# Kernel tuning notes

Measured on AMD Instinct MI355X. Metric: run time of the kernel, lower is better.

Reference implementation:

```python
import jax, jax.numpy as jnp
import numpy as np

DIM = 180
HEADS = 6
HEAD_DIM = DIM // HEADS
SCALE = HEAD_DIM ** (-0.5)
BW, N, K = 8192, 64, 16


def setup_inputs() -> dict:
    key = jax.random.key(0)
    ks = jax.random.split(key, 6)
    return {
        "x": jax.random.normal(ks[0], (BW, N, DIM), dtype=jnp.float32),
        "bpe_windows": jax.random.normal(ks[1], (BW, N, K), dtype=jnp.float32),
        "qkv_w": jax.random.normal(ks[2], (3 * DIM, DIM), dtype=jnp.float32) * 0.05,
        "qkv_b": jax.random.normal(ks[3], (3 * DIM,), dtype=jnp.float32) * 0.05,
        "proj_w": jax.random.normal(ks[4], (DIM, DIM), dtype=jnp.float32) * 0.05,
        "proj_b": jax.random.normal(ks[5], (DIM,), dtype=jnp.float32) * 0.05,
        "tau": jnp.ones((HEADS, 1, 1), dtype=jnp.float32),
    }


def reference(x, bpe_windows, qkv_w, qkv_b, proj_w, proj_b, tau):
    B_, n, C = x.shape
    # qkv projection -> (3, B_, H, N, hd)
    qkv = (x @ qkv_w.T + qkv_b).reshape(B_, n, 3, HEADS, HEAD_DIM)
    qkv = jnp.transpose(qkv, (2, 0, 3, 1, 4))
    q, k, v = qkv[0], qkv[1], qkv[2]
    q = q * SCALE
    attn = jnp.einsum("bhid,bhjd->bhij", q, k)  # (B_, H, N, N)
    # geodesic bias from BPE embeddings: d_B(i,j) = ||bpe_i - bpe_j||_2
    diff = bpe_windows[:, :, None, :] - bpe_windows[:, None, :, :]  # (B_, N, N, K)
    d_B = jnp.sqrt(jnp.sum(diff * diff, axis=-1))  # (B_, N, N)
    log_W_geo = -d_B[:, None, :, :] / jnp.clip(tau, 1e-6)[None]  # (B_, H, N, N)
    attn = jax.nn.softmax(attn + log_W_geo, axis=-1)
    out = jnp.einsum("bhij,bhjd->bhid", attn, v)  # (B_, H, N, hd)
    out = jnp.transpose(out, (0, 2, 1, 3)).reshape(B_, n, C)
    return out @ proj_w.T + proj_b
```

## Files before the change

### kernel.cpp

```cpp
#include <hip/hip_runtime.h>
#include <hip/hip_fp16.h>
#include <math.h>

typedef __attribute__((ext_vector_type(8))) short short8b;
typedef __attribute__((ext_vector_type(4))) float f32x4;
typedef __attribute__((ext_vector_type(4))) unsigned short ushort4b;
typedef __attribute__((ext_vector_type(2))) unsigned short ushort2b;

#define NWIN 8192
#define NT   1024
#define SCALE 0.18257418583505536f

#define XB_P 200
#define QK_P 200
#define VT_P 72
#define DB_P 68
#define OFF_XB  0
#define OFF_QK  25600
#define OFF_VT  51200
#define OFF_DB  65024
#define OFF_BPE 73728
#define LDS_BYTES 78848

#define WK 192
#define ATT_P 184

__device__ __forceinline__ unsigned short f2bf(float f) {
    union { float f; unsigned int u; } v; v.f = f;
    return (unsigned short)((v.u + 0x7FFFu + ((v.u >> 16) & 1u)) >> 16);
}

__global__ void prep_weights(const float* __restrict__ qkv_w,
                             const float* __restrict__ proj_w,
                             unsigned short* __restrict__ wq2,
                             unsigned short* __restrict__ wp)
{
    const int idx = blockIdx.x * 256 + threadIdx.x;
    if (idx < 2 * 270 * WK) {
        const int p = idx / (270 * WK);
        const int rr = (idx / WK) % 270;
        const int kcol = idx % WK;
        const int which = rr / 90, hh = (rr % 90) / 30, dd = rr % 30;
        const int r_orig = which * 180 + (3 * p + hh) * 30 + dd;
        wq2[idx] = f2bf((kcol < 180) ? qkv_w[r_orig * 180 + kcol] : 0.f);
    }
    const int j = idx - 2 * 270 * WK;
    if (j >= 0 && j < WK * WK) {
        const int r = j / WK, c = j % WK;
        wp[j] = f2bf((r < 180 && c < 180) ? proj_w[r * 180 + c] : 0.f);
    }
}

__global__ void __launch_bounds__(NT, 8)
waga_mfma(const float* __restrict__ x,
          const float* __restrict__ bpe,
          const unsigned short* __restrict__ wq2,
          const unsigned short* __restrict__ wp,
          const float* __restrict__ qkv_b,
          const float* __restrict__ proj_b,
          const float* __restrict__ tau,
          float* __restrict__ out)
{
    extern __shared__ char smem[];
    unsigned short* xb   = (unsigned short*)(smem + OFF_XB);
    unsigned short* qk3  = (unsigned short*)(smem + OFF_QK);
    unsigned short* vT3  = (unsigned short*)(smem + OFF_VT);
    unsigned short* dBs  = (unsigned short*)(smem + OFF_DB);
    float*          bpes = (float*)(smem + OFF_BPE);

    const int b = blockIdx.x;
    const int t = threadIdx.x;
    const int w = t >> 6;
    const int l = t & 63;
    const int lr = l & 15;
    const int g  = l >> 4;

    unsigned short* attg = (unsigned short*)((char*)out + (size_t)b * 46080 + 22528);

    if (t < 192) {
        const int n = t / 3, c = t % 3;
        ushort4b z = {0, 0, 0, 0};
        *reinterpret_cast<ushort4b*>(xb + n * XB_P + 180 + 4 * c) = z;
    } else if (t < 576) {
        const int i = t - 192;
        const int n = i / 6, r = i % 6;
        const int col = (r >> 1) * 64 + (r & 1) * 32 + 30;
        ushort2b z2 = {0, 0};
        *reinterpret_cast<ushort2b*>(qk3 + n * QK_P + col) = z2;
    } else if (t < 640) {
        const int n = t - 576;
        ushort4b z = {0, 0, 0, 0};
        *reinterpret_cast<ushort4b*>(attg + n * ATT_P + 180) = z;
    }
    {
        const float* xw = x + (size_t)b * 11520;
        for (int i = t; i < 64 * 45; i += NT) {
            const int n = i / 45, c4 = i % 45;
            const float4 v = *reinterpret_cast<const float4*>(xw + i * 4);
            ushort4b o;
            o[0] = f2bf(v.x); o[1] = f2bf(v.y); o[2] = f2bf(v.z); o[3] = f2bf(v.w);
            *reinterpret_cast<ushort4b*>(xb + n * XB_P + c4 * 4) = o;
        }
    }
    if (t < 256) {
        const float4 v = *reinterpret_cast<const float4*>(bpe + (size_t)b * 1024 + t * 4);
        *reinterpret_cast<float4*>(bpes + (t >> 2) * 20 + (t & 3) * 4) = v;
    }
    __syncthreads();

    {
        const int ti = t >> 4, tj = t & 15;
        float acc[4] = {0.f, 0.f, 0.f, 0.f};
        #pragma unroll
        for (int k4 = 0; k4 < 4; ++k4) {
            const float4 a = *reinterpret_cast<const float4*>(bpes + ti * 20 + 4 * k4);
            #pragma unroll
            for (int e = 0; e < 4; ++e) {
                const float4 bb = *reinterpret_cast<const float4*>(bpes + (tj + 16 * e) * 20 + 4 * k4);
                float d;
                d = a.x - bb.x; acc[e] += d * d;
                d = a.y - bb.y; acc[e] += d * d;
                d = a.z - bb.z; acc[e] += d * d;
                d = a.w - bb.w; acc[e] += d * d;
            }
        }
        #pragma unroll
        for (int e = 0; e < 4; ++e)
            dBs[ti * DB_P + tj + 16 * e] =
                __half_as_ushort(__float2half_rn(sqrtf(acc[e])));
    }

    for (int pass = 0; pass < 2; ++pass) {
        if (pass) __syncthreads();

        const unsigned short* wqp = wq2 + (size_t)pass * 270 * WK;
        for (int tile = w; tile < 18; tile += 16) {
            const int seg = tile >> 1;
            const int which = seg / 3, hh = seg % 3;
            const int wbase = which * 90 + hh * 30;
            const int ddr = ((tile & 1) << 4) + lr;
            const bool arow_ok = (ddr < 30);
            const int ddb = ((tile & 1) << 4) + (g << 2);
            const int bbase = which * 180 + (3 * pass + hh) * 30 + ddb;
            float bias[4];
            #pragma unroll
            for (int i = 0; i < 4; ++i)
                bias[i] = (ddb + i < 30) ? qkv_b[bbase + i] : 0.f;
            f32x4 acc[4];
            #pragma unroll
            for (int mt = 0; mt < 4; ++mt) {
                acc[mt][0] = bias[0]; acc[mt][1] = bias[1];
                acc[mt][2] = bias[2]; acc[mt][3] = bias[3];
            }
            #pragma unroll
            for (int kk = 0; kk < 6; ++kk) {
                short8b af;
                if (arow_ok)
                    af = *reinterpret_cast<const short8b*>(
                        wqp + (size_t)(wbase + ddr) * WK + kk * 32 + g * 8);
                else
                    af = short8b{0,0,0,0,0,0,0,0};
                #pragma unroll
                for (int mt = 0; mt < 4; ++mt) {
                    const short8b bf = *reinterpret_cast<const short8b*>(
                        xb + (mt * 16 + lr) * XB_P + kk * 32 + g * 8);
                    acc[mt] = __builtin_amdgcn_mfma_f32_16x16x32_bf16(af, bf, acc[mt], 0, 0, 0);
                }
            }
            #pragma unroll
            for (int mt = 0; mt < 4; ++mt) {
                const int tok = mt * 16 + lr;
                float v0 = acc[mt][0], v1 = acc[mt][1], v2 = acc[mt][2], v3 = acc[mt][3];
                if (which == 0) { v0 *= SCALE; v1 *= SCALE; v2 *= SCALE; v3 *= SCALE; }
                if (which < 2) {
                    unsigned short* dst = qk3 + tok * QK_P + hh * 64 + which * 32 + ddb;
                    if (ddb < 28) {
                        ushort4b o = { f2bf(v0), f2bf(v1), f2bf(v2), f2bf(v3) };
                        *reinterpret_cast<ushort4b*>(dst) = o;
                    } else {
                        ushort2b o = { f2bf(v0), f2bf(v1) };
                        *reinterpret_cast<ushort2b*>(dst) = o;
                    }
                } else {
                    const int c = (tok & 32) + ((tok >> 2) & 3) * 8 + ((tok >> 4) & 1) * 4 + (tok & 3);
                    unsigned short* base = vT3 + hh * 2304 + c;
                    if (ddb + 0 < 30) base[(ddb + 0) * VT_P] = f2bf(v0);
                    if (ddb + 1 < 30) base[(ddb + 1) * VT_P] = f2bf(v1);
                    if (ddb + 2 < 30) base[(ddb + 2) * VT_P] = f2bf(v2);
                    if (ddb + 3 < 30) base[(ddb + 3) * VT_P] = f2bf(v3);
                }
            }
        }
        __syncthreads();

        if (w < 12) {
            const int hh = w >> 2, mt = w & 3;
            const int h = 3 * pass + hh;
            const float itau = 1.f / fmaxf(tau[h], 1e-6f);
            f32x4 s[4];
            #pragma unroll
            for (int jt = 0; jt < 4; ++jt)
                #pragma unroll
                for (int i = 0; i < 4; ++i) {
                    const float d = __half2float(__ushort_as_half(
                        dBs[(jt * 16 + g * 4 + i) * DB_P + mt * 16 + lr]));
                    s[jt][i] = -d * itau;
                }
            const short8b qf = *reinterpret_cast<const short8b*>(
                qk3 + (mt * 16 + lr) * QK_P + hh * 64 + g * 8);
            #pragma unroll
            for (int jt = 0; jt < 4; ++jt) {
                const short8b kf = *reinterpret_cast<const short8b*>(
                    qk3 + (jt * 16 + lr) * QK_P + hh * 64 + 32 + g * 8);
                s[jt] = __builtin_amdgcn_mfma_f32_16x16x32_bf16(kf, qf, s[jt], 0, 0, 0);
            }
            float mx = s[0][0];
            #pragma unroll
            for (int jt = 0; jt < 4; ++jt)
                #pragma unroll
                for (int i = 0; i < 4; ++i) mx = fmaxf(mx, s[jt][i]);
            mx = fmaxf(mx, __shfl_xor(mx, 16));
            mx = fmaxf(mx, __shfl_xor(mx, 32));
            float sum = 0.f;
            #pragma unroll
            for (int jt = 0; jt < 4; ++jt)
                #pragma unroll
                for (int i = 0; i < 4; ++i) {
                    const float p = __expf(s[jt][i] - mx);
                    s[jt][i] = p; sum += p;
                }
            sum += __shfl_xor(sum, 16);
            sum += __shfl_xor(sum, 32);
            const float inv = 1.f / sum;
            short8b pb[2];
            #pragma unroll
            for (int ks = 0; ks < 2; ++ks) {
                pb[ks][0] = (short)f2bf(s[2 * ks][0] * inv);
                pb[ks][1] = (short)f2bf(s[2 * ks][1] * inv);
                pb[ks][2] = (short)f2bf(s[2 * ks][2] * inv);
                pb[ks][3] = (short)f2bf(s[2 * ks][3] * inv);
                pb[ks][4] = (short)f2bf(s[2 * ks + 1][0] * inv);
                pb[ks][5] = (short)f2bf(s[2 * ks + 1][1] * inv);
                pb[ks][6] = (short)f2bf(s[2 * ks + 1][2] * inv);
                pb[ks][7] = (short)f2bf(s[2 * ks + 1][3] * inv);
            }
            const int tok = mt * 16 + lr;
            #pragma unroll
            for (int ntd = 0; ntd < 2; ++ntd) {
                f32x4 o = {0.f, 0.f, 0.f, 0.f};
                #pragma unroll
                for (int ks = 0; ks < 2; ++ks) {
                    const short8b va = *reinterpret_cast<const short8b*>(
                        vT3 + hh * 2304 + (ntd * 16 + lr) * VT_P + ks * 32 + g * 8);
                    o = __builtin_amdgcn_mfma_f32_16x16x32_bf16(va, pb[ks], o, 0, 0, 0);
                }
                const int col = h * 30 + ntd * 16 + g * 4;
                unsigned short* dst = attg + tok * ATT_P + col;
                if (ntd == 0 || g < 3) {
                    ushort4b ov = { f2bf(o[0]), f2bf(o[1]), f2bf(o[2]), f2bf(o[3]) };
                    *reinterpret_cast<ushort4b*>(dst) = ov;
                } else {
                    ushort2b ov = { f2bf(o[0]), f2bf(o[1]) };
                    *reinterpret_cast<ushort2b*>(dst) = ov;
                }
            }
        }
    }
    __syncthreads();

    f32x4 pacc[3];
    #pragma unroll
    for (int q3 = 0; q3 < 3; ++q3) {
        const int tid = 3 * w + q3;
        const int nt = tid >> 2, mt = tid & 3;
        f32x4 acc = {0.f, 0.f, 0.f, 0.f};
        #pragma unroll
        for (int kk = 0; kk < 6; ++kk) {
            short8b af;
            if (kk == 5 && g == 3)
                af = short8b{0,0,0,0,0,0,0,0};
            else
                af = *reinterpret_cast<const short8b*>(
                    attg + (mt * 16 + lr) * ATT_P + kk * 32 + g * 8);
            const short8b bf = *reinterpret_cast<const short8b*>(
                wp + (nt * 16 + lr) * WK + kk * 32 + g * 8);
            acc = __builtin_amdgcn_mfma_f32_16x16x32_bf16(af, bf, acc, 0, 0, 0);
        }
        pacc[q3] = acc;
    }
    __syncthreads();
    #pragma unroll
    for (int q3 = 0; q3 < 3; ++q3) {
        const int tid = 3 * w + q3;
        const int nt = tid >> 2, mt = tid & 3;
        const int chan = nt * 16 + lr;
        if (chan < 180) {
            const float pbv = proj_b[chan];
            #pragma unroll
            for (int i = 0; i < 4; ++i)
                out[((size_t)b * 64 + mt * 16 + g * 4 + i) * 180 + chan] = pacc[q3][i] + pbv;
        }
    }
}

extern "C" void kernel_launch(void* const* d_in, const int* in_sizes, int n_in,
                              void* d_out, int out_size, void* d_ws, size_t ws_size,
                              hipStream_t stream) {
    (void)in_sizes; (void)n_in; (void)out_size; (void)ws_size;
    const float* x      = (const float*)d_in[0];
    const float* bpe    = (const float*)d_in[1];
    const float* qkv_w  = (const float*)d_in[2];
    const float* qkv_b  = (const float*)d_in[3];
    const float* proj_w = (const float*)d_in[4];
    const float* proj_b = (const float*)d_in[5];
    const float* tau    = (const float*)d_in[6];

    unsigned short* wq2 = (unsigned short*)d_ws;
    unsigned short* wp  = wq2 + 2 * 270 * WK;

    prep_weights<<<(2 * 270 * WK + WK * WK + 255) / 256, 256, 0, stream>>>(
        qkv_w, proj_w, wq2, wp);

    (void)hipFuncSetAttribute((const void*)waga_mfma,
                              hipFuncAttributeMaxDynamicSharedMemorySize,
                              LDS_BYTES);
    waga_mfma<<<NWIN, NT, LDS_BYTES, stream>>>(x, bpe, wq2, wp, qkv_b, proj_b, tau,
                                               (float*)d_out);
}
```

Measured before the change: 799.7 us.

## Compute all six heads in one pass with LDS-resident attention output

Replaces the two-pass, three-heads-per-pass schedule with a single pass that projects Q/K/V for all six heads into a larger LDS buffer, removing one barrier round and the repeated work. The per-head attention output, previously spilled to the global output buffer as scratch, now goes into LDS (reusing the x buffer), and the projection weights are padded per head so the output projection reads 32-wide head slots directly. Weight and operand fragments are preloaded and double-buffered in registers, the distance matrix is kept in fp32, and final stores become float4. LDS grows from about 77KB to about 122KB, which cuts resident blocks per CU, and launch bounds change accordingly.

```diff
diff --git a/kernel.cpp b/kernel.cpp
--- a/kernel.cpp
+++ b/kernel.cpp
@@ -1,29 +1,27 @@
 #include <hip/hip_runtime.h>
-#include <hip/hip_fp16.h>
 #include <math.h>
 
 typedef __attribute__((ext_vector_type(8))) short short8b;
 typedef __attribute__((ext_vector_type(4))) float f32x4;
 typedef __attribute__((ext_vector_type(4))) unsigned short ushort4b;
-typedef __attribute__((ext_vector_type(2))) unsigned short ushort2b;
 
 #define NWIN 8192
 #define NT   1024
 #define SCALE 0.18257418583505536f
 
 #define XB_P 200
-#define QK_P 200
+#define QK_P 392
 #define VT_P 72
-#define DB_P 68
+#define DB_P 66
+
 #define OFF_XB  0
 #define OFF_QK  25600
-#define OFF_VT  51200
-#define OFF_DB  65024
-#define OFF_BPE 73728
-#define LDS_BYTES 78848
+#define OFF_VT  75776
+#define OFF_DB  103424
+#define OFF_BPE 120320
+#define LDS_BYTES 125440
 
 #define WK 192
-#define ATT_P 184
 
 __device__ __forceinline__ unsigned short f2bf(float f) {
     union { float f; unsigned int u; } v; v.f = f;
@@ -32,30 +30,35 @@
 
 __global__ void prep_weights(const float* __restrict__ qkv_w,
                              const float* __restrict__ proj_w,
-                             unsigned short* __restrict__ wq2,
-                             unsigned short* __restrict__ wp)
+                             unsigned short* __restrict__ wqr,
+                             unsigned short* __restrict__ wpr)
 {
     const int idx = blockIdx.x * 256 + threadIdx.x;
-    if (idx < 2 * 270 * WK) {
-        const int p = idx / (270 * WK);
-        const int rr = (idx / WK) % 270;
-        const int kcol = idx % WK;
-        const int which = rr / 90, hh = (rr % 90) / 30, dd = rr % 30;
-        const int r_orig = which * 180 + (3 * p + hh) * 30 + dd;
-        wq2[idx] = f2bf((kcol < 180) ? qkv_w[r_orig * 180 + kcol] : 0.f);
-    }
-    const int j = idx - 2 * 270 * WK;
+    if (idx < 540 * WK) {
+        const int r = idx / WK, k = idx % WK;
+        const int seg = r / 30, dd = r % 30;
+        const int which = seg / 6, hh = seg % 6;
+        float v = 0.f;
+        if (k < 180)
+            v = qkv_w[(which * 180 + hh * 30 + dd) * 180 + k];
+        wqr[idx] = f2bf(v);
+    }
+    const int j = idx - 540 * WK;
     if (j >= 0 && j < WK * WK) {
-        const int r = j / WK, c = j % WK;
-        wp[j] = f2bf((r < 180 && c < 180) ? proj_w[r * 180 + c] : 0.f);
+        const int r = j / WK, kp = j % WK;
+        const int hh = kp >> 5, dd = kp & 31;
+        float v = 0.f;
+        if (r < 180 && dd < 30)
+            v = proj_w[r * 180 + hh * 30 + dd];
+        wpr[j] = f2bf(v);
     }
 }
 
-__global__ void __launch_bounds__(NT, 8)
+__global__ void __launch_bounds__(NT, 4)
 waga_mfma(const float* __restrict__ x,
           const float* __restrict__ bpe,
-          const unsigned short* __restrict__ wq2,
-          const unsigned short* __restrict__ wp,
+          const unsigned short* __restrict__ wqr,
+          const unsigned short* __restrict__ wpr,
           const float* __restrict__ qkv_b,
           const float* __restrict__ proj_b,
           const float* __restrict__ tau,
@@ -63,10 +66,11 @@
 {
     extern __shared__ char smem[];
     unsigned short* xb   = (unsigned short*)(smem + OFF_XB);
-    unsigned short* qk3  = (unsigned short*)(smem + OFF_QK);
-    unsigned short* vT3  = (unsigned short*)(smem + OFF_VT);
-    unsigned short* dBs  = (unsigned short*)(smem + OFF_DB);
+    unsigned short* qk   = (unsigned short*)(smem + OFF_QK);
+    unsigned short* vT   = (unsigned short*)(smem + OFF_VT);
+    float*          dBs  = (float*)(smem + OFF_DB);
     float*          bpes = (float*)(smem + OFF_BPE);
+    unsigned short* att  = xb;
 
     const int b = blockIdx.x;
     const int t = threadIdx.x;
@@ -75,22 +79,9 @@
     const int lr = l & 15;
     const int g  = l >> 4;
 
-    unsigned short* attg = (unsigned short*)((char*)out + (size_t)b * 46080 + 22528);
-
     if (t < 192) {
         const int n = t / 3, c = t % 3;
-        ushort4b z = {0, 0, 0, 0};
-        *reinterpret_cast<ushort4b*>(xb + n * XB_P + 180 + 4 * c) = z;
-    } else if (t < 576) {
-        const int i = t - 192;
-        const int n = i / 6, r = i % 6;
-        const int col = (r >> 1) * 64 + (r & 1) * 32 + 30;
-        ushort2b z2 = {0, 0};
-        *reinterpret_cast<ushort2b*>(qk3 + n * QK_P + col) = z2;
-    } else if (t < 640) {
-        const int n = t - 576;
-        ushort4b z = {0, 0, 0, 0};
-        *reinterpret_cast<ushort4b*>(attg + n * ATT_P + 180) = z;
+        *reinterpret_cast<uint2*>(xb + n * XB_P + 180 + 4 * c) = make_uint2(0u, 0u);
     }
     {
         const float* xw = x + (size_t)b * 11520;
@@ -126,179 +117,166 @@
         }
         #pragma unroll
         for (int e = 0; e < 4; ++e)
-            dBs[ti * DB_P + tj + 16 * e] =
-                __half_as_ushort(__float2half_rn(sqrtf(acc[e])));
-    }
-
-    for (int pass = 0; pass < 2; ++pass) {
-        if (pass) __syncthreads();
-
-        const unsigned short* wqp = wq2 + (size_t)pass * 270 * WK;
-        for (int tile = w; tile < 18; tile += 16) {
-            const int seg = tile >> 1;
-            const int which = seg / 3, hh = seg % 3;
-            const int wbase = which * 90 + hh * 30;
-            const int ddr = ((tile & 1) << 4) + lr;
-            const bool arow_ok = (ddr < 30);
-            const int ddb = ((tile & 1) << 4) + (g << 2);
-            const int bbase = which * 180 + (3 * pass + hh) * 30 + ddb;
-            float bias[4];
+            dBs[ti * DB_P + tj + 16 * e] = sqrtf(acc[e]);
+    }
+
+    for (int tile = w; tile < 36; tile += 16) {
+        const int seg = tile >> 1, half = tile & 1;
+        const int which = seg / 6, hh = seg % 6;
+        const int ddr = half * 16 + lr;
+        const bool arow_ok = (ddr < 30);
+        const unsigned short* wrow = wqr + (size_t)(seg * 30 + (arow_ok ? ddr : 0)) * WK;
+        short8b wf[6];
+        #pragma unroll
+        for (int kk = 0; kk < 6; ++kk) {
+            if (arow_ok)
+                wf[kk] = *reinterpret_cast<const short8b*>(wrow + kk * 32 + g * 8);
+            else
+                wf[kk] = short8b{0, 0, 0, 0, 0, 0, 0, 0};
+        }
+        const int ddb = half * 16 + g * 4;
+        const int cbase = which * 180 + hh * 30;
+        f32x4 binit;
+        #pragma unroll
+        for (int i = 0; i < 4; ++i)
+            binit[i] = (ddb + i < 30) ? qkv_b[cbase + ddb + i] : 0.f;
+        f32x4 acc[4] = {binit, binit, binit, binit};
+        short8b xf[4];
+        #pragma unroll
+        for (int mt = 0; mt < 4; ++mt)
+            xf[mt] = *reinterpret_cast<const short8b*>(xb + (mt * 16 + lr) * XB_P + g * 8);
+        #pragma unroll
+        for (int kk = 0; kk < 6; ++kk) {
+            short8b xc[4];
+            #pragma unroll
+            for (int mt = 0; mt < 4; ++mt) xc[mt] = xf[mt];
+            if (kk < 5) {
+                #pragma unroll
+                for (int mt = 0; mt < 4; ++mt)
+                    xf[mt] = *reinterpret_cast<const short8b*>(
+                        xb + (mt * 16 + lr) * XB_P + (kk + 1) * 32 + g * 8);
+            }
+            #pragma unroll
+            for (int mt = 0; mt < 4; ++mt)
+                acc[mt] = __builtin_amdgcn_mfma_f32_16x16x32_bf16(wf[kk], xc[mt], acc[mt], 0, 0, 0);
+        }
+        #pragma unroll
+        for (int mt = 0; mt < 4; ++mt) {
+            const int tok = mt * 16 + lr;
+            float v0 = acc[mt][0], v1 = acc[mt][1], v2 = acc[mt][2], v3 = acc[mt][3];
+            if (which == 0) { v0 *= SCALE; v1 *= SCALE; v2 *= SCALE; v3 *= SCALE; }
+            if (which < 2) {
+                ushort4b o;
+                o[0] = f2bf(v0); o[1] = f2bf(v1); o[2] = f2bf(v2); o[3] = f2bf(v3);
+                *reinterpret_cast<ushort4b*>(qk + tok * QK_P + hh * 64 + which * 32 + ddb) = o;
+            } else {
+                const int c = (tok & 32) + ((tok >> 2) & 3) * 8 + ((tok >> 4) & 1) * 4 + (tok & 3);
+                unsigned short* vb = vT + hh * 2304 + ddb * VT_P + c;
+                vb[0 * VT_P] = f2bf(v0);
+                vb[1 * VT_P] = f2bf(v1);
+                vb[2 * VT_P] = f2bf(v2);
+                vb[3 * VT_P] = f2bf(v3);
+            }
+        }
+    }
+    __syncthreads();
+
+    for (int u = w; u < 24; u += 16) {
+        const int h = u >> 2, mt = u & 3;
+        const unsigned short* qkh = qk + h * 64;
+        const short8b qf = *reinterpret_cast<const short8b*>(qkh + (mt * 16 + lr) * QK_P + g * 8);
+        short8b kf[4];
+        #pragma unroll
+        for (int jt = 0; jt < 4; ++jt)
+            kf[jt] = *reinterpret_cast<const short8b*>(qkh + (jt * 16 + lr) * QK_P + 32 + g * 8);
+        short8b vf[2][2];
+        #pragma unroll
+        for (int ntd = 0; ntd < 2; ++ntd)
+            #pragma unroll
+            for (int ks = 0; ks < 2; ++ks)
+                vf[ntd][ks] = *reinterpret_cast<const short8b*>(
+                    vT + h * 2304 + (ntd * 16 + lr) * VT_P + ks * 32 + g * 8);
+        const float itau = 1.f / fmaxf(tau[h], 1e-6f);
+        f32x4 s[4];
+        #pragma unroll
+        for (int jt = 0; jt < 4; ++jt)
             #pragma unroll
             for (int i = 0; i < 4; ++i)
-                bias[i] = (ddb + i < 30) ? qkv_b[bbase + i] : 0.f;
-            f32x4 acc[4];
-            #pragma unroll
-            for (int mt = 0; mt < 4; ++mt) {
-                acc[mt][0] = bias[0]; acc[mt][1] = bias[1];
-                acc[mt][2] = bias[2]; acc[mt][3] = bias[3];
-            }
-            #pragma unroll
-            for (int kk = 0; kk < 6; ++kk) {
-                short8b af;
-                if (arow_ok)
-                    af = *reinterpret_cast<const short8b*>(
-                        wqp + (size_t)(wbase + ddr) * WK + kk * 32 + g * 8);
-                else
-                    af = short8b{0,0,0,0,0,0,0,0};
-                #pragma unroll
-                for (int mt = 0; mt < 4; ++mt) {
-                    const short8b bf = *reinterpret_cast<const short8b*>(
-                        xb + (mt * 16 + lr) * XB_P + kk * 32 + g * 8);
-                    acc[mt] = __builtin_amdgcn_mfma_f32_16x16x32_bf16(af, bf, acc[mt], 0, 0, 0);
-                }
-            }
-            #pragma unroll
-            for (int mt = 0; mt < 4; ++mt) {
+                s[jt][i] = -itau * dBs[(jt * 16 + g * 4 + i) * DB_P + mt * 16 + lr];
+        #pragma unroll
+        for (int jt = 0; jt < 4; ++jt)
+            s[jt] = __builtin_amdgcn_mfma_f32_16x16x32_bf16(kf[jt], qf, s[jt], 0, 0, 0);
+        float mx = s[0][0];
+        #pragma unroll
+        for (int jt = 0; jt < 4; ++jt)
+            #pragma unroll
+            for (int i = 0; i < 4; ++i) mx = fmaxf(mx, s[jt][i]);
+        mx = fmaxf(mx, __shfl_xor(mx, 16));
+        mx = fmaxf(mx, __shfl_xor(mx, 32));
+        float sum = 0.f;
+        #pragma unroll
+        for (int jt = 0; jt < 4; ++jt)
+            #pragma unroll
+            for (int i = 0; i < 4; ++i) {
+                const float p = __expf(s[jt][i] - mx);
+                s[jt][i] = p; sum += p;
+            }
+        sum += __shfl_xor(sum, 16);
+        sum += __shfl_xor(sum, 32);
+        const float inv = 1.f / sum;
+        short8b pb[2];
+        #pragma unroll
+        for (int ks = 0; ks < 2; ++ks) {
+            pb[ks][0] = (short)f2bf(s[2 * ks][0] * inv);
+            pb[ks][1] = (short)f2bf(s[2 * ks][1] * inv);
+            pb[ks][2] = (short)f2bf(s[2 * ks][2] * inv);
+            pb[ks][3] = (short)f2bf(s[2 * ks][3] * inv);
+            pb[ks][4] = (short)f2bf(s[2 * ks + 1][0] * inv);
+            pb[ks][5] = (short)f2bf(s[2 * ks + 1][1] * inv);
+            pb[ks][6] = (short)f2bf(s[2 * ks + 1][2] * inv);
+            pb[ks][7] = (short)f2bf(s[2 * ks + 1][3] * inv);
+        }
+        const int tok = mt * 16 + lr;
+        #pragma unroll
+        for (int ntd = 0; ntd < 2; ++ntd) {
+            f32x4 o = {0.f, 0.f, 0.f, 0.f};
+            o = __builtin_amdgcn_mfma_f32_16x16x32_bf16(vf[ntd][0], pb[0], o, 0, 0, 0);
+            o = __builtin_amdgcn_mfma_f32_16x16x32_bf16(vf[ntd][1], pb[1], o, 0, 0, 0);
+            ushort4b ov;
+            ov[0] = f2bf(o[0]); ov[1] = f2bf(o[1]); ov[2] = f2bf(o[2]); ov[3] = f2bf(o[3]);
+            *reinterpret_cast<ushort4b*>(att + tok * XB_P + h * 32 + ntd * 16 + g * 4) = ov;
+        }
+    }
+    __syncthreads();
+
+    {
+        const int mt = w & 3, ntb = w >> 2;
+        short8b attf[6];
+        #pragma unroll
+        for (int kk = 0; kk < 6; ++kk)
+            attf[kk] = *reinterpret_cast<const short8b*>(
+                att + (mt * 16 + lr) * XB_P + kk * 32 + g * 8);
+        #pragma unroll
+        for (int q3 = 0; q3 < 3; ++q3) {
+            const int nt = ntb + 4 * q3;
+            const unsigned short* wrow = wpr + (size_t)(nt * 16 + lr) * WK;
+            short8b wf[6];
+            #pragma unroll
+            for (int kk = 0; kk < 6; ++kk)
+                wf[kk] = *reinterpret_cast<const short8b*>(wrow + kk * 32 + g * 8);
+            const int cb = nt * 16 + g * 4;
+            f32x4 acc;
+            #pragma unroll
+            for (int i = 0; i < 4; ++i)
+                acc[i] = (cb + i < 180) ? proj_b[cb + i] : 0.f;
+            #pragma unroll
+            for (int kk = 0; kk < 6; ++kk)
+                acc = __builtin_amdgcn_mfma_f32_16x16x32_bf16(wf[kk], attf[kk], acc, 0, 0, 0);
+            if (cb < 177) {
                 const int tok = mt * 16 + lr;
-                float v0 = acc[mt][0], v1 = acc[mt][1], v2 = acc[mt][2], v3 = acc[mt][3];
-                if (which == 0) { v0 *= SCALE; v1 *= SCALE; v2 *= SCALE; v3 *= SCALE; }
-                if (which < 2) {
-                    unsigned short* dst = qk3 + tok * QK_P + hh * 64 + which * 32 + ddb;
-                    if (ddb < 28) {
-                        ushort4b o = { f2bf(v0), f2bf(v1), f2bf(v2), f2bf(v3) };
-                        *reinterpret_cast<ushort4b*>(dst) = o;
-                    } else {
-                        ushort2b o = { f2bf(v0), f2bf(v1) };
-                        *reinterpret_cast<ushort2b*>(dst) = o;
-                    }
-                } else {
-                    const int c = (tok & 32) + ((tok >> 2) & 3) * 8 + ((tok >> 4) & 1) * 4 + (tok & 3);
-                    unsigned short* base = vT3 + hh * 2304 + c;
-                    if (ddb + 0 < 30) base[(ddb + 0) * VT_P] = f2bf(v0);
-                    if (ddb + 1 < 30) base[(ddb + 1) * VT_P] = f2bf(v1);
-                    if (ddb + 2 < 30) base[(ddb + 2) * VT_P] = f2bf(v2);
-                    if (ddb + 3 < 30) base[(ddb + 3) * VT_P] = f2bf(v3);
-                }
-            }
-        }
-        __syncthreads();
-
-        if (w < 12) {
-            const int hh = w >> 2, mt = w & 3;
-            const int h = 3 * pass + hh;
-            const float itau = 1.f / fmaxf(tau[h], 1e-6f);
-            f32x4 s[4];
-            #pragma unroll
-            for (int jt = 0; jt < 4; ++jt)
-                #pragma unroll
-                for (int i = 0; i < 4; ++i) {
-                    const float d = __half2float(__ushort_as_half(
-                        dBs[(jt * 16 + g * 4 + i) * DB_P + mt * 16 + lr]));
-                    s[jt][i] = -d * itau;
-                }
-            const short8b qf = *reinterpret_cast<const short8b*>(
-                qk3 + (mt * 16 + lr) * QK_P + hh * 64 + g * 8);
-            #pragma unroll
-            for (int jt = 0; jt < 4; ++jt) {
-                const short8b kf = *reinterpret_cast<const short8b*>(
-                    qk3 + (jt * 16 + lr) * QK_P + hh * 64 + 32 + g * 8);
-                s[jt] = __builtin_amdgcn_mfma_f32_16x16x32_bf16(kf, qf, s[jt], 0, 0, 0);
-            }
-            float mx = s[0][0];
-            #pragma unroll
-            for (int jt = 0; jt < 4; ++jt)
-                #pragma unroll
-                for (int i = 0; i < 4; ++i) mx = fmaxf(mx, s[jt][i]);
-            mx = fmaxf(mx, __shfl_xor(mx, 16));
-            mx = fmaxf(mx, __shfl_xor(mx, 32));
-            float sum = 0.f;
-            #pragma unroll
-            for (int jt = 0; jt < 4; ++jt)
-                #pragma unroll
-                for (int i = 0; i < 4; ++i) {
-                    const float p = __expf(s[jt][i] - mx);
-                    s[jt][i] = p; sum += p;
-                }
-            sum += __shfl_xor(sum, 16);
-            sum += __shfl_xor(sum, 32);
-            const float inv = 1.f / sum;
-            short8b pb[2];
-            #pragma unroll
-            for (int ks = 0; ks < 2; ++ks) {
-                pb[ks][0] = (short)f2bf(s[2 * ks][0] * inv);
-                pb[ks][1] = (short)f2bf(s[2 * ks][1] * inv);
-                pb[ks][2] = (short)f2bf(s[2 * ks][2] * inv);
-                pb[ks][3] = (short)f2bf(s[2 * ks][3] * inv);
-                pb[ks][4] = (short)f2bf(s[2 * ks + 1][0] * inv);
-                pb[ks][5] = (short)f2bf(s[2 * ks + 1][1] * inv);
-                pb[ks][6] = (short)f2bf(s[2 * ks + 1][2] * inv);
-                pb[ks][7] = (short)f2bf(s[2 * ks + 1][3] * inv);
-            }
-            const int tok = mt * 16 + lr;
-            #pragma unroll
-            for (int ntd = 0; ntd < 2; ++ntd) {
-                f32x4 o = {0.f, 0.f, 0.f, 0.f};
-                #pragma unroll
-                for (int ks = 0; ks < 2; ++ks) {
-                    const short8b va = *reinterpret_cast<const short8b*>(
-                        vT3 + hh * 2304 + (ntd * 16 + lr) * VT_P + ks * 32 + g * 8);
-                    o = __builtin_amdgcn_mfma_f32_16x16x32_bf16(va, pb[ks], o, 0, 0, 0);
-                }
-                const int col = h * 30 + ntd * 16 + g * 4;
-                unsigned short* dst = attg + tok * ATT_P + col;
-                if (ntd == 0 || g < 3) {
-                    ushort4b ov = { f2bf(o[0]), f2bf(o[1]), f2bf(o[2]), f2bf(o[3]) };
-                    *reinterpret_cast<ushort4b*>(dst) = ov;
-                } else {
-                    ushort2b ov = { f2bf(o[0]), f2bf(o[1]) };
-                    *reinterpret_cast<ushort2b*>(dst) = ov;
-                }
-            }
-        }
-    }
-    __syncthreads();
-
-    f32x4 pacc[3];
-    #pragma unroll
-    for (int q3 = 0; q3 < 3; ++q3) {
-        const int tid = 3 * w + q3;
-        const int nt = tid >> 2, mt = tid & 3;
-        f32x4 acc = {0.f, 0.f, 0.f, 0.f};
-        #pragma unroll
-        for (int kk = 0; kk < 6; ++kk) {
-            short8b af;
-            if (kk == 5 && g == 3)
-                af = short8b{0,0,0,0,0,0,0,0};
-            else
-                af = *reinterpret_cast<const short8b*>(
-                    attg + (mt * 16 + lr) * ATT_P + kk * 32 + g * 8);
-            const short8b bf = *reinterpret_cast<const short8b*>(
-                wp + (nt * 16 + lr) * WK + kk * 32 + g * 8);
-            acc = __builtin_amdgcn_mfma_f32_16x16x32_bf16(af, bf, acc, 0, 0, 0);
-        }
-        pacc[q3] = acc;
-    }
-    __syncthreads();
-    #pragma unroll
-    for (int q3 = 0; q3 < 3; ++q3) {
-        const int tid = 3 * w + q3;
-        const int nt = tid >> 2, mt = tid & 3;
-        const int chan = nt * 16 + lr;
-        if (chan < 180) {
-            const float pbv = proj_b[chan];
-            #pragma unroll
-            for (int i = 0; i < 4; ++i)
-                out[((size_t)b * 64 + mt * 16 + g * 4 + i) * 180 + chan] = pacc[q3][i] + pbv;
+                *reinterpret_cast<float4*>(out + ((size_t)b * 64 + tok) * 180 + cb) =
+                    make_float4(acc[0], acc[1], acc[2], acc[3]);
+            }
         }
     }
 }
@@ -315,15 +293,15 @@
     const float* proj_b = (const float*)d_in[5];
     const float* tau    = (const float*)d_in[6];
 
-    unsigned short* wq2 = (unsigned short*)d_ws;
-    unsigned short* wp  = wq2 + 2 * 270 * WK;
-
-    prep_weights<<<(2 * 270 * WK + WK * WK + 255) / 256, 256, 0, stream>>>(
-        qkv_w, proj_w, wq2, wp);
+    unsigned short* wqr = (unsigned short*)d_ws;
+    unsigned short* wpr = wqr + 540 * WK;
+
+    prep_weights<<<(540 * WK + WK * WK + 255) / 256, 256, 0, stream>>>(
+        qkv_w, proj_w, wqr, wpr);
 
     (void)hipFuncSetAttribute((const void*)waga_mfma,
                               hipFuncAttributeMaxDynamicSharedMemorySize,
                               LDS_BYTES);
-    waga_mfma<<<NWIN, NT, LDS_BYTES, stream>>>(x, bpe, wq2, wp, qkv_b, proj_b, tau,
+    waga_mfma<<<NWIN, NT, LDS_BYTES, stream>>>(x, bpe, wqr, wpr, qkv_b, proj_b, tau,
                                                (float*)d_out);
 }
```

Measured after the change: 745.1 us. -6.8%, faster.
